# Optimization experiments

Hardware: AMD Instinct MI355X
Metric: run time of the kernel (lower is better)

The kernel has to match this reference:

```python
import jax, jax.numpy as jnp
import numpy as np


def setup_inputs() -> dict:
    key = jax.random.key(0)
    ks = jax.random.split(key, 7)
    B, S, D, F, E = 4, 2048, 1024, 4096, 8
    scale = 0.02
    return {
        "x": jax.random.normal(ks[0], (B, S, D), dtype=jnp.float32),
        "gate_w": jax.random.normal(ks[1], (D, E), dtype=jnp.float32) * scale,
        "gate_b": jnp.zeros((E,), dtype=jnp.float32),
        "w1": jax.random.normal(ks[2], (E, D, F), dtype=jnp.float32) * scale,
        "b1": jnp.zeros((E, F), dtype=jnp.float32),
        "w2": jax.random.normal(ks[3], (E, F, D), dtype=jnp.float32) * scale,
        "b2": jnp.zeros((E, D), dtype=jnp.float32),
        "top_k": 2,
    }


def reference(x, gate_w, gate_b, w1, b1, w2, b2, top_k):
    B, S, D = x.shape
    E = w1.shape[0]
    xf = x.reshape(-1, D)                      # [T, D], T = B*S
    T = xf.shape[0]

    # Router: top-k logits, softmax over the selected k (as in torch code)
    logits = xf @ gate_w + gate_b              # [T, E]
    rw, sel = jax.lax.top_k(logits, top_k)     # [T, k], [T, k]
    w = jax.nn.softmax(rw, axis=-1)            # [T, k]

    # Dense combine weights: combine[t, e] = sum_k w[t,k] * (sel[t,k]==e)
    combine = jnp.zeros((T, E), dtype=xf.dtype)
    combine = combine.at[jnp.arange(T)[:, None], sel].add(w)

    # Loop over small fixed expert count; each expert FFN on all tokens,
    # weighted by combine (zero for unrouted tokens). Dropout p honored as 0 (eval).
    out = jnp.zeros_like(xf)
    for e in range(E):
        h = jax.nn.gelu(xf @ w1[e] + b1[e], approximate=False)  # torch F.gelu = exact
        out = out + combine[:, e:e + 1] * (h @ w2[e] + b2[e])
    return out.reshape(B, S, D)
```

## Files before the change

kernel.cpp:

```cpp
#include <hip/hip_runtime.h>
#include <math.h>

#define T_TOK 8192
#define DDIM  1024
#define FDIM  4096
#define NEXP  8
#define MT256 72
#define NSLOT (2 * T_TOK)
#define NG1   (16 * MT256)
#define NG2   (8 * MT256)

typedef __attribute__((ext_vector_type(8))) short short8;
typedef __attribute__((ext_vector_type(4))) float f32x4;
typedef unsigned short u16;
typedef unsigned int   u32;

typedef const __attribute__((address_space(1))) u32* gp_t;
typedef       __attribute__((address_space(3))) u32* lp_t;

__device__ __forceinline__ void gload16(const void* g, void* l) {
  __builtin_amdgcn_global_load_lds((gp_t)g, (lp_t)l, 16, 0, 0);
}

#define VM2 asm volatile("s_waitcnt vmcnt(2)" ::: "memory")
#define VM0 asm volatile("s_waitcnt vmcnt(0)" ::: "memory")
#define SBAR __builtin_amdgcn_s_barrier()
#define SCHED0 __builtin_amdgcn_sched_barrier(0)

__device__ __forceinline__ u16 f2bf(float f) {
  u32 u = __float_as_uint(f);
  u = u + 0x7FFFu + ((u >> 16) & 1u);
  return (u16)(u >> 16);
}

__device__ __forceinline__ int imin(int a, int b) { return a < b ? a : b; }

__device__ __forceinline__ float gelu_fast(float v) {
  float u = 0.7978845608f * (v + 0.044715f * v * v * v);
  float t2 = __expf(2.f * u);
  float th = 1.f - 2.f / (t2 + 1.f);
  return 0.5f * v * (1.f + th);
}

__device__ __forceinline__ int xcd_swz(int orig, int nwg) {
  int xcd = orig & 7;
  int q = nwg >> 3, r = nwg & 7;
  int base = (xcd < r) ? xcd * (q + 1) : r * (q + 1) + (xcd - r) * q;
  return base + (orig >> 3);
}

__device__ void wtrans_tile(float* __restrict__ tile,
                            const float* __restrict__ in, u16* __restrict__ out,
                            int M, int N, int r0, int c0)
{
  const int tid = threadIdx.x;
  const int tr = tid >> 4, tc = (tid & 15) * 4;
  #pragma unroll
  for (int p = 0; p < 4; p++) {
    int r = p * 16 + tr;
    float4 v = *(const float4*)(in + (size_t)(r0 + r) * N + (c0 + tc));
    tile[r * 65 + tc]     = v.x; tile[r * 65 + tc + 1] = v.y;
    tile[r * 65 + tc + 2] = v.z; tile[r * 65 + tc + 3] = v.w;
  }
  __syncthreads();
  const int oc = tid >> 3, om = (tid & 7) * 8;
  #pragma unroll
  for (int p = 0; p < 2; p++) {
    int c = p * 32 + oc;
    short8 o;
    #pragma unroll
    for (int j = 0; j < 8; j++) o[j] = (short)f2bf(tile[(om + j) * 65 + c]);
    *(short8*)(out + (size_t)(c0 + c) * M + (r0 + om)) = o;
  }
}

__global__ __launch_bounds__(256) void prep_kernel(
    const float* __restrict__ x, const float* __restrict__ gw,
    const float* __restrict__ gb, u16* __restrict__ xb,
    int* __restrict__ counts, int* __restrict__ sel, float* __restrict__ wts,
    const float* __restrict__ w1, u16* __restrict__ w1t,
    const float* __restrict__ w2, u16* __restrict__ w2t)
{
  __shared__ __align__(16) float tile[64 * 65];
  const int b = blockIdx.x;
  if (b < 16384) {
    if (b < 8192) {
      int e = b >> 10, rem = b & 1023;
      int tm = rem >> 4, tn = rem & 15;
      wtrans_tile(tile, w2 + (size_t)e * FDIM * DDIM,
                  w2t + (size_t)e * FDIM * DDIM, FDIM, DDIM, tm * 64, tn * 64);
    } else {
      int tt = b - 8192;
      int e = tt >> 10, rem = tt & 1023;
      int tn = rem >> 4, tm = rem & 15;
      wtrans_tile(tile, w1 + (size_t)e * DDIM * FDIM,
                  w1t + (size_t)e * DDIM * FDIM, DDIM, FDIM, tm * 64, tn * 64);
    }
    return;
  }
  const int t    = (b - 16384) * 4 + (threadIdx.x >> 6);
  const int lane = threadIdx.x & 63;
  const float* xr = x + (size_t)t * DDIM;
  u16* xbr = xb + (size_t)t * DDIM;
  float lg[NEXP];
  #pragma unroll
  for (int e = 0; e < NEXP; e++) lg[e] = 0.f;
  #pragma unroll
  for (int i = 0; i < 4; i++) {
    int d0 = i * 256 + lane * 4;
    float4 v = *(const float4*)(xr + d0);
    ushort4 o;
    o.x = f2bf(v.x); o.y = f2bf(v.y); o.z = f2bf(v.z); o.w = f2bf(v.w);
    *(ushort4*)(xbr + d0) = o;
    const float* g = gw + (size_t)d0 * NEXP;
    #pragma unroll
    for (int e = 0; e < NEXP; e++)
      lg[e] += v.x * g[e] + v.y * g[NEXP + e] + v.z * g[2 * NEXP + e] + v.w * g[3 * NEXP + e];
  }
  #pragma unroll
  for (int off = 32; off > 0; off >>= 1) {
    #pragma unroll
    for (int e = 0; e < NEXP; e++) lg[e] += __shfl_down(lg[e], off);
  }
  if (lane == 0) {
    float v0 = -1e30f, v1 = -1e30f; int s0 = 0, s1 = 0;
    #pragma unroll
    for (int e = 0; e < NEXP; e++) {
      float v = lg[e] + gb[e];
      if (v > v0) { v1 = v0; s1 = s0; v0 = v; s0 = e; }
      else if (v > v1) { v1 = v; s1 = e; }
    }
    float a  = expf(v1 - v0);
    float w0 = 1.f / (1.f + a);
    sel[t * 2] = s0; sel[t * 2 + 1] = s1;
    wts[t * 2] = w0; wts[t * 2 + 1] = 1.f - w0;
    atomicAdd(&counts[s0], 1); atomicAdd(&counts[s1], 1);
  }
}

__global__ __launch_bounds__(1024) void scan_assign_kernel(
    const int* __restrict__ counts, const int* __restrict__ sel,
    const float* __restrict__ wts,
    int* __restrict__ offsets, int* __restrict__ map_e, int* __restrict__ map_r,
    int* __restrict__ nT, int* __restrict__ stok, float* __restrict__ swgt)
{
  __shared__ int spos[NEXP];
  if (threadIdx.x == 0) {
    int run = 0, nt = 0;
    for (int e = 0; e < NEXP; e++) {
      offsets[e] = run; spos[e] = run;
      int c = counts[e];
      int ntile = (c + 255) >> 8;
      for (int i = 0; i < ntile; i++) { map_e[nt] = e; map_r[nt] = i * 256; nt++; }
      run += c;
    }
    nT[0] = nt;
  }
  __syncthreads();
  for (int t = threadIdx.x; t < T_TOK; t += 1024) {
    #pragma unroll
    for (int k = 0; k < 2; k++) {
      int e = sel[t * 2 + k];
      int p = atomicAdd(&spos[e], 1);
      stok[p] = t; swgt[p] = wts[t * 2 + k];
    }
  }
}

__global__ __launch_bounds__(1024, 4) void gemm1_kernel(
    const u16* __restrict__ xb, const int* __restrict__ slot_token,
    const u16* __restrict__ W1T, const float* __restrict__ B1,
    const int* __restrict__ counts, const int* __restrict__ offsets,
    const int* __restrict__ map_e, const int* __restrict__ map_r,
    const int* __restrict__ nT, u16* __restrict__ H)
{
  __shared__ __align__(16) char lds[3 * 32768];
  const int L     = xcd_swz(blockIdx.x, NG1);
  const int xg    = L / 144;
  const int local = L - xg * 144;
  const int tl    = local >> 4;
  const int n_idx = local & 15;
  const int t_idx = xg * 9 + tl;
  if (t_idx >= nT[0]) return;
  const int e    = map_e[t_idx];
  const int row0 = map_r[t_idx];
  const int cnt  = counts[e];
  const int off  = offsets[e];
  const int n0   = n_idx * 256;

  const int tid = threadIdx.x, wave = tid >> 6, lane = tid & 63;
  const int lr = lane & 15, lq = lane >> 4;
  const int wr = wave >> 2, wc = wave & 3;
  const int l2 = lane >> 2, lb = (lane & 3) * 16;

  const int R = wave * 16 + l2;
  int tok = slot_token[imin(off + row0 + R, NSLOT - 1)];
  if ((u32)tok >= T_TOK) tok = 0;
  const char* gA = (const char*)xb + (size_t)tok * 2048 + lb;
  const char* gB = (const char*)W1T + (size_t)(e * FDIM + n0 + R) * 2048 + lb;

  auto stage = [&](int slot, int k0) {
    char* base = lds + slot * 32768;
    gload16(gA + k0, base + wave * 1024 + lane * 16);
    gload16(gB + k0, base + 16384 + wave * 1024 + lane * 16);
  };

  f32x4 acc[4][4] = {};
  auto compute = [&](int slot) {
    const u16* As = (const u16*)(lds + slot * 32768);
    const u16* Bs = (const u16*)(lds + slot * 32768 + 16384);
    short8 a[4], bf[4];
    #pragma unroll
    for (int m = 0; m < 4; m++)
      a[m] = *(const short8*)&As[(wr * 64 + m * 16 + lr) * 32 + lq * 8];
    #pragma unroll
    for (int n = 0; n < 4; n++)
      bf[n] = *(const short8*)&Bs[(wc * 64 + n * 16 + lr) * 32 + lq * 8];
    #pragma unroll
    for (int m = 0; m < 4; m++)
      #pragma unroll
      for (int n = 0; n < 4; n++)
        acc[m][n] = __builtin_amdgcn_mfma_f32_16x16x32_bf16(a[m], bf[n], acc[m][n], 0, 0, 0);
  };

  stage(0, 0); stage(1, 64);
  VM2; SCHED0; SBAR; SCHED0;
  #pragma unroll 1
  for (int t = 0; t < 32; t++) {
    if (t + 2 < 32) stage((t + 2) % 3, (t + 2) * 64);
    compute(t % 3);
    SCHED0;
    if (t + 2 < 32)       { VM2; }
    else if (t + 2 == 32) { VM0; }
    SCHED0; SBAR; SCHED0;
  }

  #pragma unroll
  for (int nn = 0; nn < 4; nn++) {
    int col = n0 + wc * 64 + nn * 16 + lr;
    float b1v = B1[e * FDIM + col];
    #pragma unroll
    for (int m = 0; m < 4; m++) {
      int rbase = wr * 64 + m * 16 + lq * 4;
      #pragma unroll
      for (int j = 0; j < 4; j++) {
        int r = rbase + j;
        if (row0 + r < cnt) {
          float v = acc[m][nn][j] + b1v;
          H[(size_t)(off + row0 + r) * FDIM + col] = f2bf(gelu_fast(v));
        }
      }
    }
  }
}

__global__ __launch_bounds__(1024, 4) void gemm2_kernel(
    const u16* __restrict__ H, const u16* __restrict__ W2T,
    const float* __restrict__ B2,
    const int* __restrict__ counts, const int* __restrict__ offsets,
    const int* __restrict__ slot_token, const float* __restrict__ slot_weight,
    const int* __restrict__ map_e, const int* __restrict__ map_r,
    const int* __restrict__ nT, float* __restrict__ out)
{
  __shared__ __align__(16) char lds[3 * 32768];
  const int L     = xcd_swz(blockIdx.x, NG2);
  const int xg    = L / 72;
  const int local = L - xg * 72;
  const int tl    = local >> 3;
  const int combo = local & 7;
  const int sp    = combo >> 2;
  const int n_idx = combo & 3;
  const int t_idx = xg * 9 + tl;
  if (t_idx >= nT[0]) return;
  const int e    = map_e[t_idx];
  const int row0 = map_r[t_idx];
  const int cnt  = counts[e];
  const int off  = offsets[e];
  const int n0   = n_idx * 256;
  const int kbase = sp * 4096;

  const int tid = threadIdx.x, wave = tid >> 6, lane = tid & 63;
  const int lr = lane & 15, lq = lane >> 4;
  const int wr = wave >> 2, wc = wave & 3;
  const int l2 = lane >> 2, lb = (lane & 3) * 16;

  const int R = wave * 16 + l2;
  int aidx = imin(off + row0 + R, NSLOT - 1);
  const char* gA = (const char*)H + (size_t)aidx * 8192 + kbase + lb;
  const char* gB = (const char*)W2T + (size_t)(e * DDIM + n0 + R) * 8192 + kbase + lb;

  auto stage = [&](int slot, int k0) {
    char* base = lds + slot * 32768;
    gload16(gA + k0, base + wave * 1024 + lane * 16);
    gload16(gB + k0, base + 16384 + wave * 1024 + lane * 16);
  };

  f32x4 acc[4][4] = {};
  auto compute = [&](int slot) {
    const u16* As = (const u16*)(lds + slot * 32768);
    const u16* Bs = (const u16*)(lds + slot * 32768 + 16384);
    short8 a[4], bf[4];
    #pragma unroll
    for (int m = 0; m < 4; m++)
      a[m] = *(const short8*)&As[(wr * 64 + m * 16 + lr) * 32 + lq * 8];
    #pragma unroll
    for (int n = 0; n < 4; n++)
      bf[n] = *(const short8*)&Bs[(wc * 64 + n * 16 + lr) * 32 + lq * 8];
    #pragma unroll
    for (int m = 0; m < 4; m++)
      #pragma unroll
      for (int n = 0; n < 4; n++)
        acc[m][n] = __builtin_amdgcn_mfma_f32_16x16x32_bf16(a[m], bf[n], acc[m][n], 0, 0, 0);
  };

  stage(0, 0); stage(1, 64);
  VM2; SCHED0; SBAR; SCHED0;
  #pragma unroll 1
  for (int t = 0; t < 64; t++) {
    if (t + 2 < 64) stage((t + 2) % 3, (t + 2) * 64);
    compute(t % 3);
    SCHED0;
    if (t + 2 < 64)       { VM2; }
    else if (t + 2 == 64) { VM0; }
    SCHED0; SBAR; SCHED0;
  }

  #pragma unroll
  for (int m = 0; m < 4; m++) {
    int rbase = wr * 64 + m * 16 + lq * 4;
    #pragma unroll
    for (int j = 0; j < 4; j++) {
      int r = rbase + j;
      if (row0 + r >= cnt) continue;
      int s = off + row0 + r;
      int tok = slot_token[s];
      float wgt = slot_weight[s];
      #pragma unroll
      for (int n = 0; n < 4; n++) {
        int col = n0 + wc * 64 + n * 16 + lr;
        float v = acc[m][n][j];
        if (sp == 0) v += B2[e * DDIM + col];
        atomicAdd(&out[(size_t)tok * DDIM + col], wgt * v);
      }
    }
  }
}

extern "C" void kernel_launch(void* const* d_in, const int* in_sizes, int n_in,
                              void* d_out, int out_size, void* d_ws, size_t ws_size,
                              hipStream_t stream)
{
  (void)in_sizes; (void)n_in; (void)ws_size;
  const float* x  = (const float*)d_in[0];
  const float* gw = (const float*)d_in[1];
  const float* gb = (const float*)d_in[2];
  const float* w1 = (const float*)d_in[3];
  const float* b1 = (const float*)d_in[4];
  const float* w2 = (const float*)d_in[5];
  const float* b2 = (const float*)d_in[6];

  char* ws = (char*)d_ws;
  int*   counts = (int*)(ws + 0);
  int*   offp   = (int*)(ws + 64);
  int*   nT     = (int*)(ws + 128);
  int*   map_e  = (int*)(ws + 256);
  int*   map_r  = (int*)(ws + 1024);

  size_t p = 2048;
  int*   sel   = (int*)(ws + p);   p += (size_t)T_TOK * 2 * 4;
  float* wts   = (float*)(ws + p); p += (size_t)T_TOK * 2 * 4;
  int*   stok  = (int*)(ws + p);   p += (size_t)NSLOT * 4;
  float* swgt  = (float*)(ws + p); p += (size_t)NSLOT * 4;
  p = (p + 1048575) & ~(size_t)1048575;
  u16*   xb    = (u16*)(ws + p);   p += (size_t)T_TOK * DDIM * 2;
  u16*   w1t   = (u16*)(ws + p);   p += (size_t)NEXP * DDIM * FDIM * 2;
  u16*   w2t   = (u16*)(ws + p);   p += (size_t)NEXP * DDIM * FDIM * 2;
  u16*   Hbuf  = (u16*)(ws + p);

  hipMemsetAsync(ws, 0, 256, stream);
  hipMemsetAsync(d_out, 0, (size_t)out_size * sizeof(float), stream);
  prep_kernel<<<16384 + T_TOK / 4, 256, 0, stream>>>(
      x, gw, gb, xb, counts, sel, wts, w1, w1t, w2, w2t);
  scan_assign_kernel<<<1, 1024, 0, stream>>>(counts, sel, wts, offp, map_e, map_r, nT, stok, swgt);
  gemm1_kernel<<<NG1, 1024, 0, stream>>>(
      xb, stok, w1t, b1, counts, offp, map_e, map_r, nT, Hbuf);
  gemm2_kernel<<<NG2, 1024, 0, stream>>>(
      Hbuf, w2t, b2, counts, offp, stok, swgt, map_e, map_r, nT, (float*)d_out);
}
```

Baseline: 780.2 us.

## Split prep into router and direct-register weight transpose kernels

Splits the fused prep kernel into a router kernel and a separate weight-transpose kernel. The transpose drops the LDS tile: each lane reads a column directly from global memory, with coalesced reads across lanes, and writes 8 packed bf16 values per store, using larger 128x64 tiles. The router stages the gate weights in LDS in transposed form so each expert's weights can be read as float4. This removes LDS round-trips and barriers from the transpose but adds one kernel launch. Each thread now issues strided scalar global reads, which may use bandwidth less efficiently than float4 loads.

```diff
diff --git a/kernel.cpp b/kernel.cpp
--- a/kernel.cpp
+++ b/kernel.cpp
@@ -49,56 +49,58 @@
   return base + (orig >> 3);
 }
 
-__device__ void wtrans_tile(float* __restrict__ tile,
-                            const float* __restrict__ in, u16* __restrict__ out,
-                            int M, int N, int r0, int c0)
-{
-  const int tid = threadIdx.x;
-  const int tr = tid >> 4, tc = (tid & 15) * 4;
-  #pragma unroll
-  for (int p = 0; p < 4; p++) {
-    int r = p * 16 + tr;
-    float4 v = *(const float4*)(in + (size_t)(r0 + r) * N + (c0 + tc));
-    tile[r * 65 + tc]     = v.x; tile[r * 65 + tc + 1] = v.y;
-    tile[r * 65 + tc + 2] = v.z; tile[r * 65 + tc + 3] = v.w;
-  }
-  __syncthreads();
-  const int oc = tid >> 3, om = (tid & 7) * 8;
-  #pragma unroll
-  for (int p = 0; p < 2; p++) {
-    int c = p * 32 + oc;
+__global__ __launch_bounds__(256) void wtrans_kernel(
+    const float* __restrict__ w1, u16* __restrict__ w1t,
+    const float* __restrict__ w2, u16* __restrict__ w2t)
+{
+  const int b = blockIdx.x;
+  const float* in; u16* out; int Min, Nin, m0, n0;
+  if (b < 4096) {
+    int e = b >> 9, rem = b & 511;
+    int tm = rem >> 4, tn = rem & 15;
+    in = w2 + (size_t)e * FDIM * DDIM; out = w2t + (size_t)e * FDIM * DDIM;
+    Min = FDIM; Nin = DDIM; m0 = tm * 128; n0 = tn * 64;
+  } else {
+    int bb = b - 4096;
+    int e = bb >> 9, rem = bb & 511;
+    int tm = rem >> 6, tn = rem & 63;
+    in = w1 + (size_t)e * DDIM * FDIM; out = w1t + (size_t)e * DDIM * FDIM;
+    Min = DDIM; Nin = FDIM; m0 = tm * 128; n0 = tn * 64;
+  }
+  const int w = threadIdx.x >> 6, l = threadIdx.x & 63;
+  const int c = n0 + l;
+  #pragma unroll 1
+  for (int it = 0; it < 4; it++) {
+    int r0 = m0 + it * 32 + w * 8;
     short8 o;
     #pragma unroll
-    for (int j = 0; j < 8; j++) o[j] = (short)f2bf(tile[(om + j) * 65 + c]);
-    *(short8*)(out + (size_t)(c0 + c) * M + (r0 + om)) = o;
-  }
-}
-
-__global__ __launch_bounds__(256) void prep_kernel(
+    for (int j = 0; j < 8; j++)
+      o[j] = (short)f2bf(in[(size_t)(r0 + j) * Nin + c]);
+    *(short8*)(out + (size_t)c * Min + r0) = o;
+  }
+}
+
+__global__ __launch_bounds__(256) void router_kernel(
     const float* __restrict__ x, const float* __restrict__ gw,
     const float* __restrict__ gb, u16* __restrict__ xb,
-    int* __restrict__ counts, int* __restrict__ sel, float* __restrict__ wts,
-    const float* __restrict__ w1, u16* __restrict__ w1t,
-    const float* __restrict__ w2, u16* __restrict__ w2t)
-{
-  __shared__ __align__(16) float tile[64 * 65];
-  const int b = blockIdx.x;
-  if (b < 16384) {
-    if (b < 8192) {
-      int e = b >> 10, rem = b & 1023;
-      int tm = rem >> 4, tn = rem & 15;
-      wtrans_tile(tile, w2 + (size_t)e * FDIM * DDIM,
-                  w2t + (size_t)e * FDIM * DDIM, FDIM, DDIM, tm * 64, tn * 64);
-    } else {
-      int tt = b - 8192;
-      int e = tt >> 10, rem = tt & 1023;
-      int tn = rem >> 4, tm = rem & 15;
-      wtrans_tile(tile, w1 + (size_t)e * DDIM * FDIM,
-                  w1t + (size_t)e * DDIM * FDIM, DDIM, FDIM, tm * 64, tn * 64);
-    }
-    return;
-  }
-  const int t    = (b - 16384) * 4 + (threadIdx.x >> 6);
+    int* __restrict__ counts, int* __restrict__ sel, float* __restrict__ wts)
+{
+  __shared__ __align__(16) float gwT[8 * 1028];
+  {
+    const int tid = threadIdx.x;
+    #pragma unroll
+    for (int q = 0; q < 4; q++) {
+      int d = q * 256 + tid;
+      float4 a = *(const float4*)(gw + (size_t)d * NEXP);
+      float4 cc = *(const float4*)(gw + (size_t)d * NEXP + 4);
+      gwT[0 * 1028 + d] = a.x; gwT[1 * 1028 + d] = a.y;
+      gwT[2 * 1028 + d] = a.z; gwT[3 * 1028 + d] = a.w;
+      gwT[4 * 1028 + d] = cc.x; gwT[5 * 1028 + d] = cc.y;
+      gwT[6 * 1028 + d] = cc.z; gwT[7 * 1028 + d] = cc.w;
+    }
+  }
+  __syncthreads();
+  const int t    = blockIdx.x * 4 + (threadIdx.x >> 6);
   const int lane = threadIdx.x & 63;
   const float* xr = x + (size_t)t * DDIM;
   u16* xbr = xb + (size_t)t * DDIM;
@@ -112,10 +114,11 @@
     ushort4 o;
     o.x = f2bf(v.x); o.y = f2bf(v.y); o.z = f2bf(v.z); o.w = f2bf(v.w);
     *(ushort4*)(xbr + d0) = o;
-    const float* g = gw + (size_t)d0 * NEXP;
-    #pragma unroll
-    for (int e = 0; e < NEXP; e++)
-      lg[e] += v.x * g[e] + v.y * g[NEXP + e] + v.z * g[2 * NEXP + e] + v.w * g[3 * NEXP + e];
+    #pragma unroll
+    for (int e = 0; e < NEXP; e++) {
+      float4 g4 = *(const float4*)&gwT[e * 1028 + d0];
+      lg[e] += v.x * g4.x + v.y * g4.y + v.z * g4.z + v.w * g4.w;
+    }
   }
   #pragma unroll
   for (int off = 32; off > 0; off >>= 1) {
@@ -379,8 +382,8 @@
 
   hipMemsetAsync(ws, 0, 256, stream);
   hipMemsetAsync(d_out, 0, (size_t)out_size * sizeof(float), stream);
-  prep_kernel<<<16384 + T_TOK / 4, 256, 0, stream>>>(
-      x, gw, gb, xb, counts, sel, wts, w1, w1t, w2, w2t);
+  router_kernel<<<T_TOK / 4, 256, 0, stream>>>(x, gw, gb, xb, counts, sel, wts);
+  wtrans_kernel<<<8192, 256, 0, stream>>>(w1, w1t, w2, w2t);
   scan_assign_kernel<<<1, 1024, 0, stream>>>(counts, sel, wts, offp, map_e, map_r, nT, stok, swgt);
   gemm1_kernel<<<NG1, 1024, 0, stream>>>(
       xb, stok, w1t, b1, counts, offp, map_e, map_r, nT, Hbuf);
```

New measurement: 850.7 us. 9.0% more time.
